# Kernel optimization log

Measured on AMD Instinct MI355X. Metric: run time of the kernel, lower is better.

## Reference

```python
import jax, jax.numpy as jnp
import numpy as np

D_MODEL = 1024
N_HEADS = 16
D_HEAD = D_MODEL // N_HEADS


def setup_inputs() -> dict:
    key = jax.random.key(0)
    ks = jax.random.split(key, 5)
    s_in = 1.0 / np.sqrt(D_MODEL)
    x = jax.random.normal(ks[0], (2, 2048, D_MODEL), dtype=jnp.float32)
    W_qkv = jax.random.uniform(ks[1], (D_MODEL, 3 * D_MODEL), jnp.float32, -s_in, s_in)
    b_qkv = jax.random.uniform(ks[2], (3 * D_MODEL,), jnp.float32, -s_in, s_in)
    W_out = jax.random.uniform(ks[3], (D_MODEL, D_MODEL), jnp.float32, -s_in, s_in)
    b_out = jax.random.uniform(ks[4], (D_MODEL,), jnp.float32, -s_in, s_in)
    return {"x": x, "W_qkv": W_qkv, "b_qkv": b_qkv, "W_out": W_out, "b_out": b_out}


def reference(x, W_qkv, b_qkv, W_out, b_out):
    B, T, C = x.shape
    qkv = x @ W_qkv + b_qkv                      # [B,T,3C]
    q, k, v = jnp.split(qkv, 3, axis=-1)
    # [B,T,C] -> [B,H,T,Dh]
    def heads(t):
        return t.reshape(B, T, N_HEADS, D_HEAD).transpose(0, 2, 1, 3)
    q, k, v = heads(q), heads(k), heads(v)
    att = jnp.einsum('bhqd,bhkd->bhqk', q, k) / np.sqrt(D_HEAD).astype(np.float32)
    causal = jnp.tril(jnp.ones((T, T), dtype=bool))  # True = keep
    att = jnp.where(causal, att, -jnp.inf)
    att = jax.nn.softmax(att, axis=-1)
    y = jnp.einsum('bhqk,bhkd->bhqd', att, v)    # [B,H,T,Dh]
    y = y.transpose(0, 2, 1, 3).reshape(B, T, C)
    y = y @ W_out + b_out
    return (y, att)
```

## Files before the change

### kernel.cpp

```cpp
#include <hip/hip_runtime.h>

#define B_ 2
#define T_ 2048
#define C_ 1024
#define H_ 16
#define DH_ 64
#define N3_ 3072
#define BT_ 4096

typedef __attribute__((ext_vector_type(4))) float f32x4;
typedef __attribute__((ext_vector_type(8))) short short8;
typedef __attribute__((ext_vector_type(4))) unsigned short us4;
typedef __attribute__((ext_vector_type(4))) unsigned int u32x4;

__device__ __forceinline__ unsigned short f2bf(float f) {
  return __builtin_bit_cast(unsigned short, (__bf16)f);
}

__device__ __forceinline__ float bf2f(unsigned short s) {
  unsigned int u = ((unsigned int)s) << 16;
  return __builtin_bit_cast(float, u);
}

__device__ __forceinline__ unsigned int cvtpk(float a, float b) {
  unsigned int r;
  asm("v_cvt_pk_bf16_f32 %0, %1, %2" : "=v"(r) : "v"(a), "v"(b));
  return r;
}

__device__ __forceinline__ void gload16(const void* g, void* l) {
  __builtin_amdgcn_global_load_lds(
      (const __attribute__((address_space(1))) unsigned int*)g,
      (__attribute__((address_space(3))) unsigned int*)l, 16, 0, 0);
}

#define QSCALE 0.1803368801111137f

__global__ __launch_bounds__(256) void prep_kernel(const float* __restrict__ x,
                                                   const float* __restrict__ W_qkv,
                                                   const float* __restrict__ W_out,
                                                   unsigned short* __restrict__ xb,
                                                   unsigned short* __restrict__ wqkvT,
                                                   unsigned short* __restrict__ woutT) {
  __shared__ float tile[32][33];
  int b = blockIdx.x;
  if (b < 4096) {
    size_t i = (size_t)b * 256 + threadIdx.x;
    float4 v = *(const float4*)(x + i * 4);
    us4 o = {f2bf(v.x), f2bf(v.y), f2bf(v.z), f2bf(v.w)};
    *(us4*)(xb + i * 4) = o;
    return;
  }
  const float* W;
  unsigned short* Wt;
  int Ncols, bx, by;
  if (b < 4096 + 3072) {
    int bb = b - 4096;
    W = W_qkv; Wt = wqkvT; Ncols = 3072; bx = bb % 96; by = bb / 96;
  } else {
    int bb = b - 7168;
    W = W_out; Wt = woutT; Ncols = 1024; bx = bb % 32; by = bb / 32;
  }
  int n0 = bx * 32, k0 = by * 32;
  int tx = threadIdx.x & 31, ty = threadIdx.x >> 5;
#pragma unroll
  for (int i = 0; i < 4; ++i) {
    int k = k0 + ty + i * 8;
    tile[ty + i * 8][tx] = W[(size_t)k * Ncols + n0 + tx];
  }
  __syncthreads();
#pragma unroll
  for (int i = 0; i < 4; ++i) {
    int n = n0 + ty + i * 8;
    Wt[(size_t)n * 1024 + k0 + tx] = f2bf(tile[tx][ty + i * 8]);
  }
}

template <int MODE, int BN>
__global__ __launch_bounds__(256) void gemm_kernel(
    const unsigned short* __restrict__ A, const unsigned short* __restrict__ Bt,
    const float* __restrict__ bias, unsigned short* __restrict__ q_ws,
    unsigned short* __restrict__ k_ws, unsigned short* __restrict__ vt_ws,
    float* __restrict__ yout) {
  __shared__ unsigned short lds_a[128 * 32];
  __shared__ unsigned short lds_b[BN * 32];
  const int tid = threadIdx.x;
  const int w = tid >> 6, l = tid & 63;
  const int m0 = blockIdx.y * 128;
  const int n0 = blockIdx.x * BN;
  const int wr = (w >> 1) * 64, wc = (w & 1) * (BN / 2);
  constexpr int NI = BN / 32;
  const int K = 1024;

  f32x4 acc[4][NI] = {};
  for (int k0 = 0; k0 < K; k0 += 32) {
    __syncthreads();
#pragma unroll
    for (int i = 0; i < 2; ++i) {
      int li = i * 256 + tid;
      int row = li >> 2, cl = li & 3, cs = cl ^ (row & 3);
      gload16((const char*)A + ((size_t)(m0 + row) * K + k0) * 2 + cs * 16,
              (char*)lds_a + li * 16);
    }
#pragma unroll
    for (int i = 0; i < BN / 64; ++i) {
      int li = i * 256 + tid;
      int row = li >> 2, cl = li & 3, cs = cl ^ (row & 3);
      gload16((const char*)Bt + ((size_t)(n0 + row) * K + k0) * 2 + cs * 16,
              (char*)lds_b + li * 16);
    }
    __syncthreads();
    short8 af[4], bfr[NI];
#pragma unroll
    for (int mi = 0; mi < 4; ++mi) {
      int m = wr + mi * 16 + (l & 15);
      af[mi] = *(const short8*)((const char*)lds_a + m * 64 + (((l >> 4) ^ (m & 3)) * 16));
    }
#pragma unroll
    for (int ni = 0; ni < NI; ++ni) {
      int n = wc + ni * 16 + (l & 15);
      bfr[ni] = *(const short8*)((const char*)lds_b + n * 64 + (((l >> 4) ^ (n & 3)) * 16));
    }
#pragma unroll
    for (int mi = 0; mi < 4; ++mi)
#pragma unroll
      for (int ni = 0; ni < NI; ++ni)
        acc[mi][ni] = __builtin_amdgcn_mfma_f32_16x16x32_bf16(af[mi], bfr[ni], acc[mi][ni], 0, 0, 0);
  }

  float bi[NI];
#pragma unroll
  for (int ni = 0; ni < NI; ++ni) bi[ni] = bias[n0 + wc + ni * 16 + (l & 15)];

  if (MODE == 1) {
#pragma unroll
    for (int mi = 0; mi < 4; ++mi) {
#pragma unroll
      for (int ni = 0; ni < NI; ++ni) {
        int n = n0 + wc + ni * 16 + (l & 15);
#pragma unroll
        for (int r = 0; r < 4; ++r) {
          int m = m0 + wr + mi * 16 + ((l >> 4) << 2) + r;
          yout[(size_t)m * 1024 + n] = acc[mi][ni][r] + bi[ni];
        }
      }
    }
  } else {
    int sec = (n0 + wc) >> 10;
#pragma unroll
    for (int mi = 0; mi < 4; ++mi) {
#pragma unroll
      for (int ni = 0; ni < NI; ++ni) {
        int n = n0 + wc + ni * 16 + (l & 15);
        int nn = n & 1023, h = nn >> 6, d = nn & 63;
        if (sec == 2) {
          int mbase = m0 + wr + mi * 16 + ((l >> 4) << 2);
          int bb = mbase >> 11, t = mbase & 2047;
          us4 o;
#pragma unroll
          for (int r = 0; r < 4; ++r) o[r] = f2bf(acc[mi][ni][r] + bi[ni]);
          *(us4*)(vt_ws + ((size_t)(bb * 16 + h) * 64 + d) * 2048 + t) = o;
        } else {
#pragma unroll
          for (int r = 0; r < 4; ++r) {
            int m = m0 + wr + mi * 16 + ((l >> 4) << 2) + r;
            int bb = m >> 11, t = m & 2047;
            float v = acc[mi][ni][r] + bi[ni];
            size_t idx = ((size_t)(bb * 16 + h) * 2048 + t) * 64 + d;
            if (sec == 0)
              q_ws[idx] = f2bf(v * QSCALE);
            else
              k_ws[idx] = f2bf(v);
          }
        }
      }
    }
  }
}

__global__ __launch_bounds__(512) void attn_kernel(
    const unsigned short* __restrict__ q_ws, const unsigned short* __restrict__ k_ws,
    const unsigned short* __restrict__ vt_ws, float* __restrict__ att,
    unsigned short* __restrict__ yh) {
  __shared__ unsigned short lds_all[2][16384];
  const int tid = threadIdx.x, w = tid >> 6, l = tid & 63;
  const int id = blockIdx.x;
  const int rr = id >> 8, j = id & 255;
  int qt = j & 15;
  if (rr) qt = 15 - qt;
  const int bh = (j >> 4) + (rr << 4);
  const int q0 = qt * 128;
  const size_t hoff = (size_t)bh * (2048 * 64);
  const char* kbase = (const char*)k_ws + hoff * 2;
  const char* vbase = (const char*)vt_ws + hoff * 2;
  float* attb = att + (size_t)bh * 2048 * 2048;

  auto stageK128 = [&](int kt, int buf) {
#pragma unroll
    for (int i = 0; i < 2; ++i) {
      int li = i * 512 + tid;
      int row = li >> 3, cl = li & 7, cs = cl ^ (row & 7);
      gload16(kbase + ((size_t)kt * 128 + row) * 128 + cs * 16, (char*)lds_all[buf] + li * 16);
    }
  };
  auto stageV128 = [&](int kt, int buf) {
#pragma unroll
    for (int i = 0; i < 2; ++i) {
      int li = i * 512 + tid;
      int row = li >> 4, cl = li & 15, cs = cl ^ (row & 15);
      gload16(vbase + (size_t)row * 4096 + kt * 256 + cs * 16,
              (char*)lds_all[buf] + 16384 + li * 16);
    }
  };

  short8 qf[2];
  {
    int row = q0 + w * 16 + (l & 15);
    const char* qb = (const char*)q_ws + (hoff + (size_t)row * 64) * 2;
    qf[0] = *(const short8*)(qb + ((l >> 4) * 16));
    qf[1] = *(const short8*)(qb + 64 + ((l >> 4) * 16));
  }

  const int qrow = q0 + w * 16 + (l & 15);
  const int kcolbase = (l >> 4) << 2;
  const int nkt = qt + 1;

  float lsum = 0.f;
  stageK128(0, 0);
  asm volatile("s_waitcnt vmcnt(0)" ::: "memory");
  __builtin_amdgcn_s_barrier();
  for (int kt = 0; kt < nkt; ++kt) {
    const int cur = kt & 1;
    if (kt + 1 < nkt) stageK128(kt + 1, cur ^ 1);
    const bool diag = (kt == qt);
    f32x4 s[8];
#pragma unroll
    for (int ni = 0; ni < 8; ++ni) s[ni] = f32x4{0.f, 0.f, 0.f, 0.f};
#pragma unroll
    for (int ni = 0; ni < 8; ++ni) {
      int jj = ni * 16 + (l & 15);
#pragma unroll
      for (int cc = 0; cc < 2; ++cc) {
        short8 kf = *(const short8*)((const char*)lds_all[cur] + jj * 128 +
                                     (((cc * 4 + (l >> 4)) ^ (jj & 7)) * 16));
        s[ni] = __builtin_amdgcn_mfma_f32_16x16x32_bf16(kf, qf[cc], s[ni], 0, 0, 0);
      }
    }
#pragma unroll
    for (int ni = 0; ni < 8; ++ni) {
#pragma unroll
      for (int r = 0; r < 4; ++r) {
        float e = __builtin_exp2f(s[ni][r]);
        if (diag) {
          int colg = kt * 128 + ni * 16 + kcolbase + r;
          if (colg > qrow) e = 0.f;
        }
        lsum += e;
      }
    }
    if (kt + 1 < nkt) {
      asm volatile("s_waitcnt vmcnt(0)" ::: "memory");
      __builtin_amdgcn_s_barrier();
    }
  }

  lsum += __shfl_xor(lsum, 16);
  lsum += __shfl_xor(lsum, 32);
  const float invl = 1.0f / lsum;

  __syncthreads();

  f32x4 yacc[4] = {};
  const int srcA = (l & 15) + ((l >> 4) & 1) * 32;
  const int srcB = srcA + 16;
  const bool hiSel = ((l >> 4) >> 1) & 1;

  stageK128(0, 0);
  stageV128(0, 0);
  asm volatile("s_waitcnt vmcnt(0)" ::: "memory");
  __builtin_amdgcn_s_barrier();
  for (int kt = 0; kt < nkt; ++kt) {
    const int cur = kt & 1;
    if (kt + 1 < nkt) { stageK128(kt + 1, cur ^ 1); stageV128(kt + 1, cur ^ 1); }
    const bool diag = (kt == qt);
    f32x4 s[8];
#pragma unroll
    for (int ni = 0; ni < 8; ++ni) s[ni] = f32x4{0.f, 0.f, 0.f, 0.f};
#pragma unroll
    for (int ni = 0; ni < 8; ++ni) {
      int jj = ni * 16 + (l & 15);
#pragma unroll
      for (int cc = 0; cc < 2; ++cc) {
        short8 kf = *(const short8*)((const char*)lds_all[cur] + jj * 128 +
                                     (((cc * 4 + (l >> 4)) ^ (jj & 7)) * 16));
        s[ni] = __builtin_amdgcn_mfma_f32_16x16x32_bf16(kf, qf[cc], s[ni], 0, 0, 0);
      }
    }
#pragma unroll
    for (int kk = 0; kk < 4; ++kk) {
      unsigned int w0a, w1a, w0b, w1b;
#pragma unroll
      for (int nn = 0; nn < 2; ++nn) {
        int ni = 2 * kk + nn;
        f32x4 p;
#pragma unroll
        for (int r = 0; r < 4; ++r) {
          float v = __builtin_exp2f(s[ni][r]) * invl;
          if (diag) {
            int colg = kt * 128 + ni * 16 + kcolbase + r;
            if (colg > qrow) v = 0.f;
          }
          p[r] = v;
        }
        *(f32x4*)(attb + (size_t)qrow * 2048 + kt * 128 + ni * 16 + kcolbase) = p;
        if (nn == 0) { w0a = cvtpk(p[0], p[1]); w1a = cvtpk(p[2], p[3]); }
        else         { w0b = cvtpk(p[0], p[1]); w1b = cvtpk(p[2], p[3]); }
      }
      unsigned int a0 = __shfl(w0a, srcA), a0x = __shfl(w0b, srcA);
      unsigned int a1 = __shfl(w1a, srcA), a1x = __shfl(w1b, srcA);
      unsigned int b0 = __shfl(w0a, srcB), b0x = __shfl(w0b, srcB);
      unsigned int b1 = __shfl(w1a, srcB), b1x = __shfl(w1b, srcB);
      u32x4 F = {hiSel ? a0x : a0, hiSel ? a1x : a1, hiSel ? b0x : b0, hiSel ? b1x : b1};
      short8 pf = __builtin_bit_cast(short8, F);
      int kc = kk * 4 + (l >> 4);
#pragma unroll
      for (int ni = 0; ni < 4; ++ni) {
        int d = ni * 16 + (l & 15);
        short8 vf = *(const short8*)((const char*)lds_all[cur] + 16384 + d * 256 +
                                     ((kc ^ (d & 15)) * 16));
        yacc[ni] = __builtin_amdgcn_mfma_f32_16x16x32_bf16(pf, vf, yacc[ni], 0, 0, 0);
      }
    }
    if (kt + 1 < nkt) {
      asm volatile("s_waitcnt vmcnt(8)" ::: "memory");
      __builtin_amdgcn_s_barrier();
    }
  }

  {
    int bb = bh >> 4, h = bh & 15;
#pragma unroll
    for (int ni = 0; ni < 4; ++ni) {
      int d = ni * 16 + (l & 15);
#pragma unroll
      for (int r = 0; r < 4; ++r) {
        int t = q0 + w * 16 + ((l >> 4) << 2) + r;
        yh[((size_t)bb * 2048 + t) * 1024 + h * 64 + d] = f2bf(yacc[ni][r]);
      }
    }
  }

  int cstart = q0 + 128;
  if (cstart < 2048) {
    int nz = 2048 - cstart;
    float4 z = make_float4(0.f, 0.f, 0.f, 0.f);
    for (int row = 0; row < 128; ++row) {
      float* dst = attb + (size_t)(q0 + row) * 2048 + cstart;
      for (int c = tid * 4; c < nz; c += 2048) *(float4*)(dst + c) = z;
    }
  }
}

extern "C" void kernel_launch(void* const* d_in, const int* in_sizes, int n_in,
                              void* d_out, int out_size, void* d_ws, size_t ws_size,
                              hipStream_t stream) {
  const float* x = (const float*)d_in[0];
  const float* W_qkv = (const float*)d_in[1];
  const float* b_qkv = (const float*)d_in[2];
  const float* W_out = (const float*)d_in[3];
  const float* b_out = (const float*)d_in[4];
  float* out = (float*)d_out;

  char* ws = (char*)d_ws;
  unsigned short* xb = (unsigned short*)(ws);
  unsigned short* wqkvT = (unsigned short*)(ws + 8388608);
  unsigned short* woutT = (unsigned short*)(ws + 14680064);
  unsigned short* q_ws = (unsigned short*)(ws + 16777216);
  unsigned short* k_ws = (unsigned short*)(ws + 25165824);
  unsigned short* vt_ws = (unsigned short*)(ws + 33554432);
  unsigned short* yh_ws = (unsigned short*)(ws + 41943040);

  float* y_out = out;
  float* att_out = out + (size_t)BT_ * C_;

  prep_kernel<<<8192, 256, 0, stream>>>(x, W_qkv, W_out, xb, wqkvT, woutT);
  gemm_kernel<0, 128><<<dim3(24, 32), 256, 0, stream>>>(xb, wqkvT, b_qkv, q_ws, k_ws, vt_ws,
                                                        nullptr);
  attn_kernel<<<512, 512, 0, stream>>>(q_ws, k_ws, vt_ws, att_out, yh_ws);
  gemm_kernel<1, 64><<<dim3(16, 32), 256, 0, stream>>>(yh_ws, woutT, b_out, nullptr, nullptr,
                                                       nullptr, y_out);
}
```

Before: 213.1 us.

## Move causal-mask zero fill of attention matrix into QKV GEMM main loop

The attention kernel no longer writes zeros to the masked upper triangle of the attention output. Instead, each QKV GEMM block zero-fills a share of the fully masked 128x128 tiles, a few rows per K iteration, interleaved with its loads. The intent is to overlap the large zero-store traffic with GEMM compute and take it off the attention kernel's critical path. The plain __syncthreads are replaced with explicit lgkmcnt/vmcnt waits so the GEMM does not wait on its own fill stores. The tile indexing is intricate, and the partial vmcnt waits rely on the stores being issued after the loads.

```diff
diff --git a/kernel.cpp b/kernel.cpp
--- a/kernel.cpp
+++ b/kernel.cpp
@@ -32,6 +32,11 @@
   __builtin_amdgcn_global_load_lds(
       (const __attribute__((address_space(1))) unsigned int*)g,
       (__attribute__((address_space(3))) unsigned int*)l, 16, 0, 0);
+}
+
+__device__ __forceinline__ void lds_barrier() {
+  asm volatile("s_waitcnt lgkmcnt(0)" ::: "memory");
+  __builtin_amdgcn_s_barrier();
 }
 
 #define QSCALE 0.1803368801111137f
@@ -81,7 +86,7 @@
     const unsigned short* __restrict__ A, const unsigned short* __restrict__ Bt,
     const float* __restrict__ bias, unsigned short* __restrict__ q_ws,
     unsigned short* __restrict__ k_ws, unsigned short* __restrict__ vt_ws,
-    float* __restrict__ yout) {
+    float* __restrict__ yout, float* __restrict__ att) {
   __shared__ unsigned short lds_a[128 * 32];
   __shared__ unsigned short lds_b[BN * 32];
   const int tid = threadIdx.x;
@@ -92,9 +97,12 @@
   constexpr int NI = BN / 32;
   const int K = 1024;
 
+  const int blk = blockIdx.y * 24 + blockIdx.x;
+  int fillRound = 0;
+
   f32x4 acc[4][NI] = {};
   for (int k0 = 0; k0 < K; k0 += 32) {
-    __syncthreads();
+    lds_barrier();
 #pragma unroll
     for (int i = 0; i < 2; ++i) {
       int li = i * 256 + tid;
@@ -109,7 +117,31 @@
       gload16((const char*)Bt + ((size_t)(n0 + row) * K + k0) * 2 + cs * 16,
               (char*)lds_b + li * 16);
     }
-    __syncthreads();
+    int todo = 0;
+    if (MODE == 0) {
+      todo = 80 - fillRound;
+      if (todo > 3) todo = 3;
+      f32x4 z = {0.f, 0.f, 0.f, 0.f};
+      for (int s = 0; s < todo; ++s) {
+        int g = blk * 5 + (fillRound + s) >> 0;
+        int rid = fillRound + s;
+        int gt = blk * 5 + rid / 16;
+        int r16 = rid & 15;
+        int bh = gt / 120, u = gt % 120;
+        int t = 0;
+        while (u >= 15 - t) { u -= 15 - t; ++t; }
+        int row = t * 128 + r16 * 8 + (tid >> 5);
+        int col = 128 * (t + 1) + u * 128 + ((tid & 31) << 2);
+        *(f32x4*)(att + ((size_t)bh * 2048 + row) * 2048 + col) = z;
+        (void)g;
+      }
+      fillRound += todo;
+    }
+    if (MODE == 0 && todo == 3)      asm volatile("s_waitcnt vmcnt(3)" ::: "memory");
+    else if (MODE == 0 && todo == 2) asm volatile("s_waitcnt vmcnt(2)" ::: "memory");
+    else if (MODE == 0 && todo == 1) asm volatile("s_waitcnt vmcnt(1)" ::: "memory");
+    else                             asm volatile("s_waitcnt vmcnt(0)" ::: "memory");
+    __builtin_amdgcn_s_barrier();
     short8 af[4], bfr[NI];
 #pragma unroll
     for (int mi = 0; mi < 4; ++mi) {
@@ -349,16 +381,6 @@
       }
     }
   }
-
-  int cstart = q0 + 128;
-  if (cstart < 2048) {
-    int nz = 2048 - cstart;
-    float4 z = make_float4(0.f, 0.f, 0.f, 0.f);
-    for (int row = 0; row < 128; ++row) {
-      float* dst = attb + (size_t)(q0 + row) * 2048 + cstart;
-      for (int c = tid * 4; c < nz; c += 2048) *(float4*)(dst + c) = z;
-    }
-  }
 }
 
 extern "C" void kernel_launch(void* const* d_in, const int* in_sizes, int n_in,
@@ -385,8 +407,8 @@
 
   prep_kernel<<<8192, 256, 0, stream>>>(x, W_qkv, W_out, xb, wqkvT, woutT);
   gemm_kernel<0, 128><<<dim3(24, 32), 256, 0, stream>>>(xb, wqkvT, b_qkv, q_ws, k_ws, vt_ws,
-                                                        nullptr);
+                                                        nullptr, att_out);
   attn_kernel<<<512, 512, 0, stream>>>(q_ws, k_ws, vt_ws, att_out, yh_ws);
   gemm_kernel<1, 64><<<dim3(16, 32), 256, 0, stream>>>(yh_ws, woutT, b_out, nullptr, nullptr,
-                                                       nullptr, y_out);
-}
+                                                       nullptr, y_out, nullptr);
+}
```

Result: slower. 224.5 us (+5.4%).

## Shrink attention query tiles to 64 rows with single-buffered LDS and 256 threads

Applied to the files above, without the earlier changes.

The attention kernel now processes 64 query rows per block with 4 waves instead of 128 rows with 8 waves, launching 1024 blocks instead of 512. The LDS double buffer is dropped in favour of a single 32 KB buffer, with a load-wait-barrier per key tile. The aim is higher occupancy and finer load balancing across the causal triangle, relying on other resident blocks to hide load latency. In exchange, K/V tiles are fetched twice as often per query row, and the prefetch overlap within a block is lost.

```diff
diff --git a/kernel.cpp b/kernel.cpp
--- a/kernel.cpp
+++ b/kernel.cpp
@@ -32,6 +32,11 @@
   __builtin_amdgcn_global_load_lds(
       (const __attribute__((address_space(1))) unsigned int*)g,
       (__attribute__((address_space(3))) unsigned int*)l, 16, 0, 0);
+}
+
+__device__ __forceinline__ void lds_barrier() {
+  asm volatile("s_waitcnt lgkmcnt(0)" ::: "memory");
+  __builtin_amdgcn_s_barrier();
 }
 
 #define QSCALE 0.1803368801111137f
@@ -178,61 +183,60 @@
   }
 }
 
-__global__ __launch_bounds__(512) void attn_kernel(
+__global__ __launch_bounds__(256) void attn_kernel(
     const unsigned short* __restrict__ q_ws, const unsigned short* __restrict__ k_ws,
     const unsigned short* __restrict__ vt_ws, float* __restrict__ att,
     unsigned short* __restrict__ yh) {
-  __shared__ unsigned short lds_all[2][16384];
+  __shared__ unsigned short lds_all[16384];
+  char* const lds = (char*)lds_all;
   const int tid = threadIdx.x, w = tid >> 6, l = tid & 63;
   const int id = blockIdx.x;
   const int rr = id >> 8, j = id & 255;
-  int qt = j & 15;
-  if (rr) qt = 15 - qt;
-  const int bh = (j >> 4) + (rr << 4);
-  const int q0 = qt * 128;
+  const int v = j & 31;
+  const int qb = (rr & 1) ? 31 - v : v;
+  const int bh = (j >> 5) | (rr << 3);
+  const int q0 = qb * 64;
   const size_t hoff = (size_t)bh * (2048 * 64);
   const char* kbase = (const char*)k_ws + hoff * 2;
   const char* vbase = (const char*)vt_ws + hoff * 2;
   float* attb = att + (size_t)bh * 2048 * 2048;
 
-  auto stageK128 = [&](int kt, int buf) {
-#pragma unroll
-    for (int i = 0; i < 2; ++i) {
-      int li = i * 512 + tid;
+  auto stageK128 = [&](int kt) {
+#pragma unroll
+    for (int i = 0; i < 4; ++i) {
+      int li = i * 256 + tid;
       int row = li >> 3, cl = li & 7, cs = cl ^ (row & 7);
-      gload16(kbase + ((size_t)kt * 128 + row) * 128 + cs * 16, (char*)lds_all[buf] + li * 16);
+      gload16(kbase + ((size_t)kt * 128 + row) * 128 + cs * 16, lds + li * 16);
     }
   };
-  auto stageV128 = [&](int kt, int buf) {
-#pragma unroll
-    for (int i = 0; i < 2; ++i) {
-      int li = i * 512 + tid;
+  auto stageV128 = [&](int kt) {
+#pragma unroll
+    for (int i = 0; i < 4; ++i) {
+      int li = i * 256 + tid;
       int row = li >> 4, cl = li & 15, cs = cl ^ (row & 15);
-      gload16(vbase + (size_t)row * 4096 + kt * 256 + cs * 16,
-              (char*)lds_all[buf] + 16384 + li * 16);
+      gload16(vbase + (size_t)row * 4096 + kt * 256 + cs * 16, lds + 16384 + li * 16);
     }
   };
 
   short8 qf[2];
   {
     int row = q0 + w * 16 + (l & 15);
-    const char* qb = (const char*)q_ws + (hoff + (size_t)row * 64) * 2;
-    qf[0] = *(const short8*)(qb + ((l >> 4) * 16));
-    qf[1] = *(const short8*)(qb + 64 + ((l >> 4) * 16));
+    const char* qb_ = (const char*)q_ws + (hoff + (size_t)row * 64) * 2;
+    qf[0] = *(const short8*)(qb_ + ((l >> 4) * 16));
+    qf[1] = *(const short8*)(qb_ + 64 + ((l >> 4) * 16));
   }
 
   const int qrow = q0 + w * 16 + (l & 15);
   const int kcolbase = (l >> 4) << 2;
-  const int nkt = qt + 1;
+  const int nkt = (qb >> 1) + 1;
 
   float lsum = 0.f;
-  stageK128(0, 0);
-  asm volatile("s_waitcnt vmcnt(0)" ::: "memory");
-  __builtin_amdgcn_s_barrier();
   for (int kt = 0; kt < nkt; ++kt) {
-    const int cur = kt & 1;
-    if (kt + 1 < nkt) stageK128(kt + 1, cur ^ 1);
-    const bool diag = (kt == qt);
+    lds_barrier();
+    stageK128(kt);
+    asm volatile("s_waitcnt vmcnt(0)" ::: "memory");
+    __builtin_amdgcn_s_barrier();
+    const bool diag = (kt == nkt - 1);
     f32x4 s[8];
 #pragma unroll
     for (int ni = 0; ni < 8; ++ni) s[ni] = f32x4{0.f, 0.f, 0.f, 0.f};
@@ -241,8 +245,7 @@
       int jj = ni * 16 + (l & 15);
 #pragma unroll
       for (int cc = 0; cc < 2; ++cc) {
-        short8 kf = *(const short8*)((const char*)lds_all[cur] + jj * 128 +
-                                     (((cc * 4 + (l >> 4)) ^ (jj & 7)) * 16));
+        short8 kf = *(const short8*)(lds + jj * 128 + (((cc * 4 + (l >> 4)) ^ (jj & 7)) * 16));
         s[ni] = __builtin_amdgcn_mfma_f32_16x16x32_bf16(kf, qf[cc], s[ni], 0, 0, 0);
       }
     }
@@ -258,31 +261,24 @@
         lsum += e;
       }
     }
-    if (kt + 1 < nkt) {
-      asm volatile("s_waitcnt vmcnt(0)" ::: "memory");
-      __builtin_amdgcn_s_barrier();
-    }
   }
 
   lsum += __shfl_xor(lsum, 16);
   lsum += __shfl_xor(lsum, 32);
   const float invl = 1.0f / lsum;
-
-  __syncthreads();
 
   f32x4 yacc[4] = {};
   const int srcA = (l & 15) + ((l >> 4) & 1) * 32;
   const int srcB = srcA + 16;
   const bool hiSel = ((l >> 4) >> 1) & 1;
 
-  stageK128(0, 0);
-  stageV128(0, 0);
-  asm volatile("s_waitcnt vmcnt(0)" ::: "memory");
-  __builtin_amdgcn_s_barrier();
   for (int kt = 0; kt < nkt; ++kt) {
-    const int cur = kt & 1;
-    if (kt + 1 < nkt) { stageK128(kt + 1, cur ^ 1); stageV128(kt + 1, cur ^ 1); }
-    const bool diag = (kt == qt);
+    lds_barrier();
+    stageK128(kt);
+    stageV128(kt);
+    asm volatile("s_waitcnt vmcnt(0)" ::: "memory");
+    __builtin_amdgcn_s_barrier();
+    const bool diag = (kt == nkt - 1);
     f32x4 s[8];
 #pragma unroll
     for (int ni = 0; ni < 8; ++ni) s[ni] = f32x4{0.f, 0.f, 0.f, 0.f};
@@ -291,8 +287,7 @@
       int jj = ni * 16 + (l & 15);
 #pragma unroll
       for (int cc = 0; cc < 2; ++cc) {
-        short8 kf = *(const short8*)((const char*)lds_all[cur] + jj * 128 +
-                                     (((cc * 4 + (l >> 4)) ^ (jj & 7)) * 16));
+        short8 kf = *(const short8*)(lds + jj * 128 + (((cc * 4 + (l >> 4)) ^ (jj & 7)) * 16));
         s[ni] = __builtin_amdgcn_mfma_f32_16x16x32_bf16(kf, qf[cc], s[ni], 0, 0, 0);
       }
     }
@@ -305,12 +300,12 @@
         f32x4 p;
 #pragma unroll
         for (int r = 0; r < 4; ++r) {
-          float v = __builtin_exp2f(s[ni][r]) * invl;
+          float vv = __builtin_exp2f(s[ni][r]) * invl;
           if (diag) {
             int colg = kt * 128 + ni * 16 + kcolbase + r;
-            if (colg > qrow) v = 0.f;
+            if (colg > qrow) vv = 0.f;
           }
-          p[r] = v;
+          p[r] = vv;
         }
         *(f32x4*)(attb + (size_t)qrow * 2048 + kt * 128 + ni * 16 + kcolbase) = p;
         if (nn == 0) { w0a = cvtpk(p[0], p[1]); w1a = cvtpk(p[2], p[3]); }
@@ -326,14 +321,9 @@
 #pragma unroll
       for (int ni = 0; ni < 4; ++ni) {
         int d = ni * 16 + (l & 15);
-        short8 vf = *(const short8*)((const char*)lds_all[cur] + 16384 + d * 256 +
-                                     ((kc ^ (d & 15)) * 16));
+        short8 vf = *(const short8*)(lds + 16384 + d * 256 + ((kc ^ (d & 15)) * 16));
         yacc[ni] = __builtin_amdgcn_mfma_f32_16x16x32_bf16(pf, vf, yacc[ni], 0, 0, 0);
       }
-    }
-    if (kt + 1 < nkt) {
-      asm volatile("s_waitcnt vmcnt(8)" ::: "memory");
-      __builtin_amdgcn_s_barrier();
     }
   }
 
@@ -350,13 +340,13 @@
     }
   }
 
-  int cstart = q0 + 128;
+  int cstart = nkt * 128;
   if (cstart < 2048) {
     int nz = 2048 - cstart;
     float4 z = make_float4(0.f, 0.f, 0.f, 0.f);
-    for (int row = 0; row < 128; ++row) {
+    for (int row = 0; row < 64; ++row) {
       float* dst = attb + (size_t)(q0 + row) * 2048 + cstart;
-      for (int c = tid * 4; c < nz; c += 2048) *(float4*)(dst + c) = z;
+      for (int c = tid * 4; c < nz; c += 1024) *(float4*)(dst + c) = z;
     }
   }
 }
@@ -386,7 +376,7 @@
   prep_kernel<<<8192, 256, 0, stream>>>(x, W_qkv, W_out, xb, wqkvT, woutT);
   gemm_kernel<0, 128><<<dim3(24, 32), 256, 0, stream>>>(xb, wqkvT, b_qkv, q_ws, k_ws, vt_ws,
                                                         nullptr);
-  attn_kernel<<<512, 512, 0, stream>>>(q_ws, k_ws, vt_ws, att_out, yh_ws);
+  attn_kernel<<<1024, 256, 0, stream>>>(q_ws, k_ws, vt_ws, att_out, yh_ws);
   gemm_kernel<1, 64><<<dim3(16, 32), 256, 0, stream>>>(yh_ws, woutT, b_out, nullptr, nullptr,
                                                        nullptr, y_out);
 }
```

After: 249.9 us. 1.17x slower.
